# Performance work log

Hardware: AMD Instinct MI355X
Metric: run time of the kernel (lower is better)

The kernel has to match this reference:

```python
import jax, jax.numpy as jnp
import numpy as np

B, DIM = 32768, 768
M, K = 128, 32          # num_subvectors, code_size
D = DIM // M            # subvector_dim = 6


def setup_inputs() -> dict:
    key = jax.random.key(0)
    kx, kc = jax.random.split(key)
    x = jax.random.normal(kx, (B, DIM), dtype=jnp.float32)
    codebooks = jax.random.normal(kc, (M, K, D), dtype=jnp.float32) * 0.01
    return {"x": x, "codebooks": codebooks}


def reference(x, codebooks):
    b = x.shape[0]
    m, k, d = codebooks.shape
    sub = x.reshape(b, m, d)                                   # (B, M, D)
    # per-subvector dot products with each code: (B, M, K)
    dots = jnp.einsum('bmd,mkd->bmk', sub, codebooks)
    soft = jax.nn.softmax(dots, axis=2)                        # (B, M, K)
    soft_q = jnp.einsum('bmk,mkd->bmd', soft, codebooks)       # (B, M, D)
    idx = jnp.argmax(dots, axis=2)                             # (B, M) int
    discrete = codebooks[jnp.arange(m)[None, :], idx]          # (B, M, D)
    # straight-through: forward = discrete, gradient flows through soft_q
    quant = soft_q - jax.lax.stop_gradient(soft_q - discrete)
    return quant.reshape(b, m * d)
```

## Files before the change

### kernel.cpp

```cpp
#include <hip/hip_runtime.h>
#include <float.h>


typedef float v2f __attribute__((ext_vector_type(2)));

#define BATCH 32768
#define DIM   768
#define K_CB  32
#define D_SUB 6
#define BROWS 16
#define RSTG  8
#define NSTG  (BROWS/RSTG)
#define HALFF 384
#define STGF  (RSTG*HALFF)
#define EPS_TIE 1e-5f

#define DPP_XOR1 0xB1
#define DPP_XOR2 0x4E

template<int CTRL>
__device__ __forceinline__ float dppf(float v) {
    return __int_as_float(__builtin_amdgcn_update_dpp(
        0, __float_as_int(v), CTRL, 0xF, 0xF, true));
}
template<int CTRL>
__device__ __forceinline__ int dppi(int v) {
    return __builtin_amdgcn_update_dpp(0, v, CTRL, 0xF, 0xF, true);
}

__device__ __forceinline__ void glds16(const float* g, float* l) {
    __builtin_amdgcn_global_load_lds(
        (const __attribute__((address_space(1))) void*)g,
        (__attribute__((address_space(3))) void*)l,
        16, 0, 0);
}

__global__ __launch_bounds__(256, 4)
void pq_head_kernel(const float* __restrict__ x,
                    const float* __restrict__ cb,
                    float* __restrict__ out) {
    __shared__ float xs[2][STGF];

    const int t     = threadIdx.x;
    const int kq    = t & 3;
    const int mloc  = t >> 2;
    const int mhalf = blockIdx.y;
    const int m     = mhalf * 64 + mloc;
    const int b0    = blockIdx.x * BROWS;

    const float* xh = x   + (size_t)mhalf * HALFF;
    float*       oh = out + (size_t)mhalf * HALFF;

    int pr[3], pc[3];
    #pragma unroll
    for (int i = 0; i < 3; ++i) {
        int f = (i * 256 + t) * 4;
        pr[i] = f / HALFF;
        pc[i] = f - pr[i] * HALFF;
    }

    #pragma unroll
    for (int i = 0; i < 3; ++i)
        glds16(xh + (size_t)(b0 + pr[i]) * DIM + pc[i],
               &xs[0][(i * 256 + t) * 4]);

    v2f cpk[4][D_SUB];
    {
        float cc[48];
        const float4* cb4 = reinterpret_cast<const float4*>(
            cb + ((size_t)m * K_CB + (size_t)kq * 8) * D_SUB);
        #pragma unroll
        for (int i = 0; i < 12; ++i) {
            float4 v = cb4[i];
            cc[4*i+0]=v.x; cc[4*i+1]=v.y; cc[4*i+2]=v.z; cc[4*i+3]=v.w;
        }
        #pragma unroll
        for (int p = 0; p < 4; ++p)
            #pragma unroll
            for (int e = 0; e < D_SUB; ++e)
                cpk[p][e] = (v2f){cc[(2*p)*D_SUB + e], cc[(2*p+1)*D_SUB + e]};
    }

    __syncthreads();

    for (int s = 0; s < NSTG; ++s) {
        float* buf = xs[s & 1];

        if (s + 1 < NSTG) {
            int rb = b0 + (s + 1) * RSTG;
            #pragma unroll
            for (int i = 0; i < 3; ++i)
                glds16(xh + (size_t)(rb + pr[i]) * DIM + pc[i],
                       &xs[(s + 1) & 1][(i * 256 + t) * 4]);
        }

        int kg8[RSTG];
        #pragma unroll
        for (int r = 0; r < RSTG; ++r) {
            const float* xr = &buf[r * HALFF + mloc * D_SUB];
            float2 x01 = *reinterpret_cast<const float2*>(xr);
            float2 x23 = *reinterpret_cast<const float2*>(xr + 2);
            float2 x45 = *reinterpret_cast<const float2*>(xr + 4);
            float xv[6] = {x01.x, x01.y, x23.x, x23.y, x45.x, x45.y};
            v2f xxe[6];
            #pragma unroll
            for (int e = 0; e < 6; ++e) xxe[e] = (v2f){xv[e], xv[e]};

            v2f acc[4];
            #pragma unroll
            for (int p = 0; p < 4; ++p) {
                v2f a = cpk[p][0] * xxe[0];
                #pragma unroll
                for (int e = 1; e < 6; ++e)
                    a = __builtin_elementwise_fma(cpk[p][e], xxe[e], a);
                acc[p] = a;
            }

            v2f t0 = __builtin_elementwise_max(acc[0], acc[1]);
            v2f t1 = __builtin_elementwise_max(acc[2], acc[3]);
            v2f t2 = __builtin_elementwise_max(t0, t1);
            float best1 = fmaxf(t2.x, t2.y);
            best1 = fmaxf(best1, dppf<DPP_XOR1>(best1));
            best1 = fmaxf(best1, dppf<DPP_XOR2>(best1));

            const float thr = best1 - EPS_TIE;
            int msk = 0;
            #pragma unroll
            for (int p = 0; p < 4; ++p) {
                if (acc[p].x > thr) msk |= 1 << (2*p);
                if (acc[p].y > thr) msk |= 1 << (2*p+1);
            }
            int full = msk << (kq * 8);
            full |= dppi<DPP_XOR1>(full);
            full |= dppi<DPP_XOR2>(full);

            int kg;
            if (__builtin_popcount(full) == 1) {
                kg = __builtin_ctz(full);
            } else {
                const float* crow = cb + (size_t)m * K_CB * D_SUB;
                double db = -1e300; int dkg = 0;
                for (int k2 = 0; k2 < K_CB; ++k2) {
                    double sa = 0.0;
                    for (int e = 0; e < 6; ++e)
                        sa = fma((double)crow[k2*6+e], (double)xv[e], sa);
                    if (sa > db) { db = sa; dkg = k2; }
                }
                kg = dkg;
            }
            kg8[r] = kg;
        }

        const bool act = (kq < 3);
        float2 gv[RSTG];
        if (act) {
            #pragma unroll
            for (int r = 0; r < RSTG; ++r)
                gv[r] = *(reinterpret_cast<const float2*>(
                    cb + ((size_t)m * K_CB + (size_t)kg8[r]) * D_SUB) + kq);
        }

        __builtin_amdgcn_sched_barrier(0);

        if (act) {
            #pragma unroll
            for (int r = 0; r < RSTG; ++r) {
                float* dst = oh + (size_t)(b0 + s * RSTG + r) * DIM + mloc * D_SUB;
                *(reinterpret_cast<float2*>(dst) + kq) = gv[r];
            }
        }

        if (s + 1 < NSTG) {
            asm volatile("s_waitcnt vmcnt(16)" ::: "memory");
            __builtin_amdgcn_s_barrier();
            __builtin_amdgcn_sched_barrier(0);
        }
    }
}

extern "C" void kernel_launch(void* const* d_in, const int* in_sizes, int n_in,
                              void* d_out, int out_size, void* d_ws, size_t ws_size,
                              hipStream_t stream) {
    const float* x  = (const float*)d_in[0];
    const float* cb = (const float*)d_in[1];
    float* out = (float*)d_out;

    dim3 grid(BATCH / BROWS, 2);
    dim3 block(256);
    hipLaunchKernelGGL(pq_head_kernel, grid, block, 0, stream, x, cb, out);
}
```

Before: 232.8 us.

## Drop in-block double buffering and process eight rows per block

Result: faster. 218.2 us (-6.3%).

```diff
diff --git a/kernel.cpp b/kernel.cpp
--- a/kernel.cpp
+++ b/kernel.cpp
@@ -8,11 +8,9 @@
 #define DIM   768
 #define K_CB  32
 #define D_SUB 6
-#define BROWS 16
-#define RSTG  8
-#define NSTG  (BROWS/RSTG)
+#define BROWS 8
 #define HALFF 384
-#define STGF  (RSTG*HALFF)
+#define STGF  (BROWS*HALFF)
 #define EPS_TIE 1e-5f
 
 #define DPP_XOR1 0xB1
@@ -39,7 +37,7 @@
 void pq_head_kernel(const float* __restrict__ x,
                     const float* __restrict__ cb,
                     float* __restrict__ out) {
-    __shared__ float xs[2][STGF];
+    __shared__ float xs[STGF];
 
     const int t     = threadIdx.x;
     const int kq    = t & 3;
@@ -51,18 +49,13 @@
     const float* xh = x   + (size_t)mhalf * HALFF;
     float*       oh = out + (size_t)mhalf * HALFF;
 
-    int pr[3], pc[3];
     #pragma unroll
     for (int i = 0; i < 3; ++i) {
         int f = (i * 256 + t) * 4;
-        pr[i] = f / HALFF;
-        pc[i] = f - pr[i] * HALFF;
+        int r = f / HALFF;
+        int c = f - r * HALFF;
+        glds16(xh + (size_t)(b0 + r) * DIM + c, &xs[f]);
     }
-
-    #pragma unroll
-    for (int i = 0; i < 3; ++i)
-        glds16(xh + (size_t)(b0 + pr[i]) * DIM + pc[i],
-               &xs[0][(i * 256 + t) * 4]);
 
     v2f cpk[4][D_SUB];
     {
@@ -83,97 +76,79 @@
 
     __syncthreads();
 
-    for (int s = 0; s < NSTG; ++s) {
-        float* buf = xs[s & 1];
+    int kg8[BROWS];
+    #pragma unroll
+    for (int r = 0; r < BROWS; ++r) {
+        const float* xr = &xs[r * HALFF + mloc * D_SUB];
+        float2 x01 = *reinterpret_cast<const float2*>(xr);
+        float2 x23 = *reinterpret_cast<const float2*>(xr + 2);
+        float2 x45 = *reinterpret_cast<const float2*>(xr + 4);
+        float xv[6] = {x01.x, x01.y, x23.x, x23.y, x45.x, x45.y};
+        v2f xxe[6];
+        #pragma unroll
+        for (int e = 0; e < 6; ++e) xxe[e] = (v2f){xv[e], xv[e]};
 
-        if (s + 1 < NSTG) {
-            int rb = b0 + (s + 1) * RSTG;
+        v2f acc[4];
+        #pragma unroll
+        for (int p = 0; p < 4; ++p) {
+            v2f a = cpk[p][0] * xxe[0];
             #pragma unroll
-            for (int i = 0; i < 3; ++i)
-                glds16(xh + (size_t)(rb + pr[i]) * DIM + pc[i],
-                       &xs[(s + 1) & 1][(i * 256 + t) * 4]);
+            for (int e = 1; e < 6; ++e)
+                a = __builtin_elementwise_fma(cpk[p][e], xxe[e], a);
+            acc[p] = a;
         }
 
-        int kg8[RSTG];
+        v2f t0 = __builtin_elementwise_max(acc[0], acc[1]);
+        v2f t1 = __builtin_elementwise_max(acc[2], acc[3]);
+        v2f t2 = __builtin_elementwise_max(t0, t1);
+        float best1 = fmaxf(t2.x, t2.y);
+        best1 = fmaxf(best1, dppf<DPP_XOR1>(best1));
+        best1 = fmaxf(best1, dppf<DPP_XOR2>(best1));
+
+        const float thr = best1 - EPS_TIE;
+        int msk = 0;
         #pragma unroll
-        for (int r = 0; r < RSTG; ++r) {
-            const float* xr = &buf[r * HALFF + mloc * D_SUB];
-            float2 x01 = *reinterpret_cast<const float2*>(xr);
-            float2 x23 = *reinterpret_cast<const float2*>(xr + 2);
-            float2 x45 = *reinterpret_cast<const float2*>(xr + 4);
-            float xv[6] = {x01.x, x01.y, x23.x, x23.y, x45.x, x45.y};
-            v2f xxe[6];
-            #pragma unroll
-            for (int e = 0; e < 6; ++e) xxe[e] = (v2f){xv[e], xv[e]};
+        for (int p = 0; p < 4; ++p) {
+            if (acc[p].x > thr) msk |= 1 << (2*p);
+            if (acc[p].y > thr) msk |= 1 << (2*p+1);
+        }
+        int full = msk << (kq * 8);
+        full |= dppi<DPP_XOR1>(full);
+        full |= dppi<DPP_XOR2>(full);
 
-            v2f acc[4];
-            #pragma unroll
-            for (int p = 0; p < 4; ++p) {
-                v2f a = cpk[p][0] * xxe[0];
-                #pragma unroll
-                for (int e = 1; e < 6; ++e)
-                    a = __builtin_elementwise_fma(cpk[p][e], xxe[e], a);
-                acc[p] = a;
+        int kg;
+        if (__builtin_popcount(full) == 1) {
+            kg = __builtin_ctz(full);
+        } else {
+            const float* crow = cb + (size_t)m * K_CB * D_SUB;
+            double db = -1e300; int dkg = 0;
+            for (int k2 = 0; k2 < K_CB; ++k2) {
+                double sa = 0.0;
+                for (int e = 0; e < 6; ++e)
+                    sa = fma((double)crow[k2*6+e], (double)xv[e], sa);
+                if (sa > db) { db = sa; dkg = k2; }
             }
+            kg = dkg;
+        }
+        kg8[r] = kg;
+    }
 
-            v2f t0 = __builtin_elementwise_max(acc[0], acc[1]);
-            v2f t1 = __builtin_elementwise_max(acc[2], acc[3]);
-            v2f t2 = __builtin_elementwise_max(t0, t1);
-            float best1 = fmaxf(t2.x, t2.y);
-            best1 = fmaxf(best1, dppf<DPP_XOR1>(best1));
-            best1 = fmaxf(best1, dppf<DPP_XOR2>(best1));
+    const bool act = (kq < 3);
+    float2 gv[BROWS];
+    if (act) {
+        #pragma unroll
+        for (int r = 0; r < BROWS; ++r)
+            gv[r] = *(reinterpret_cast<const float2*>(
+                cb + ((size_t)m * K_CB + (size_t)kg8[r]) * D_SUB) + kq);
+    }
 
-            const float thr = best1 - EPS_TIE;
-            int msk = 0;
-            #pragma unroll
-            for (int p = 0; p < 4; ++p) {
-                if (acc[p].x > thr) msk |= 1 << (2*p);
-                if (acc[p].y > thr) msk |= 1 << (2*p+1);
-            }
-            int full = msk << (kq * 8);
-            full |= dppi<DPP_XOR1>(full);
-            full |= dppi<DPP_XOR2>(full);
+    __builtin_amdgcn_sched_barrier(0);
 
-            int kg;
-            if (__builtin_popcount(full) == 1) {
-                kg = __builtin_ctz(full);
-            } else {
-                const float* crow = cb + (size_t)m * K_CB * D_SUB;
-                double db = -1e300; int dkg = 0;
-                for (int k2 = 0; k2 < K_CB; ++k2) {
-                    double sa = 0.0;
-                    for (int e = 0; e < 6; ++e)
-                        sa = fma((double)crow[k2*6+e], (double)xv[e], sa);
-                    if (sa > db) { db = sa; dkg = k2; }
-                }
-                kg = dkg;
-            }
-            kg8[r] = kg;
-        }
-
-        const bool act = (kq < 3);
-        float2 gv[RSTG];
-        if (act) {
-            #pragma unroll
-            for (int r = 0; r < RSTG; ++r)
-                gv[r] = *(reinterpret_cast<const float2*>(
-                    cb + ((size_t)m * K_CB + (size_t)kg8[r]) * D_SUB) + kq);
-        }
-
-        __builtin_amdgcn_sched_barrier(0);
-
-        if (act) {
-            #pragma unroll
-            for (int r = 0; r < RSTG; ++r) {
-                float* dst = oh + (size_t)(b0 + s * RSTG + r) * DIM + mloc * D_SUB;
-                *(reinterpret_cast<float2*>(dst) + kq) = gv[r];
-            }
-        }
-
-        if (s + 1 < NSTG) {
-            asm volatile("s_waitcnt vmcnt(16)" ::: "memory");
-            __builtin_amdgcn_s_barrier();
-            __builtin_amdgcn_sched_barrier(0);
+    if (act) {
+        #pragma unroll
+        for (int r = 0; r < BROWS; ++r) {
+            float* dst = oh + (size_t)(b0 + r) * DIM + mloc * D_SUB;
+            *(reinterpret_cast<float2*>(dst) + kq) = gv[r];
         }
     }
 }
```
